# Kernel optimization log

Measured on AMD Instinct MI355X. Metric: run time of the kernel, lower is better.

Reference implementation:

```python
import jax, jax.numpy as jnp
import numpy as np

MERGE_COEFF = 0.5  # fixed beta-merge coefficient (init arg)


def setup_inputs() -> dict:
    key = jax.random.key(0)
    k1, k2, k3, k4 = jax.random.split(key, 4)
    N, M, H = 8192, 8192, 512
    s = 1.0 / np.sqrt(H)
    return {
        "features": jax.random.normal(k1, (N, H), dtype=jnp.float32),
        "memory_features": jax.random.normal(k2, (M, H), dtype=jnp.float32),
        "Wq": jax.random.normal(k3, (H, H), dtype=jnp.float32) * s,
        "bq": jnp.zeros((H,), dtype=jnp.float32),
        "Wk": jax.random.normal(k4, (H, H), dtype=jnp.float32) * s,
        "bk": jnp.zeros((H,), dtype=jnp.float32),
    }


def reference(features, memory_features, Wq, bq, Wk, bk):
    tau = 1.0
    # torch nn.Linear: y = x @ W.T + b
    q = features @ Wq.T + bq                 # [N, H]
    k = memory_features @ Wk.T + bk          # [M, H]
    attn = jax.nn.softmax((q @ k.T) / tau, axis=-1)  # [N, M]
    augment = attn @ memory_features          # [N, H]
    c = MERGE_COEFF
    return c * features + (1.0 - c) * augment
```

## Files before the change

### kernel.cpp

```cpp
#include <hip/hip_runtime.h>


typedef _Float16 half8 __attribute__((ext_vector_type(8)));
typedef _Float16 half4 __attribute__((ext_vector_type(4)));
typedef float floatx4 __attribute__((ext_vector_type(4)));

#define MFMA16(a, b, c) __builtin_amdgcn_mfma_f32_16x16x32_f16((a), (b), (c), 0, 0, 0)

static constexpr int H = 512;
static constexpr int NROWS = 8192;

__device__ __forceinline__ void dma16(half8* lds_dst, const void* g_src) {
    __builtin_amdgcn_global_load_lds(
        (const __attribute__((address_space(1))) unsigned int*)g_src,
        (__attribute__((address_space(3))) unsigned int*)lds_dst,
        16, 0, 0);
}

__global__ void castpack_kernel(const float* __restrict__ F, const float* __restrict__ Mem,
                                const float* __restrict__ wq, const float* __restrict__ wk,
                                _Float16* __restrict__ f16pk, _Float16* __restrict__ m16pk,
                                _Float16* __restrict__ wq16, _Float16* __restrict__ wk16,
                                half8* __restrict__ vp) {
    if (blockIdx.x < 1024) {
        __shared__ _Float16 xl[16 * 520];
        const int t = threadIdx.x;
        const int rowt0 = blockIdx.x * 16;
        const float* src = (rowt0 < 8192) ? (F + (size_t)rowt0 * 512)
                                          : (Mem + (size_t)(rowt0 - 8192) * 512);
        _Float16* dstpk = (rowt0 < 8192) ? f16pk : m16pk;
        const int rowb = blockIdx.x & 511;
#pragma unroll
        for (int i = 0; i < 8; ++i) {
            int li = t + i * 256;
            int r  = li >> 7;
            int c4 = (li & 127) * 4;
            float4 v = *(const float4*)&src[(size_t)r * 512 + c4];
            half4 h;
            h[0] = (_Float16)v.x; h[1] = (_Float16)v.y;
            h[2] = (_Float16)v.z; h[3] = (_Float16)v.w;
            *(half4*)&xl[r * 520 + c4] = h;
        }
        __syncthreads();
        half8* dst = (half8*)dstpk;
#pragma unroll
        for (int i = 0; i < 4; ++i) {
            int u = t + i * 256;
            int j = u >> 4, ri = u & 15;
            half8 v = *(const half8*)&xl[ri * 520 + j * 8];
            dst[(size_t)rowb * 1024 + u] = v;
        }
    } else if (blockIdx.x < 1536) {
        size_t i4 = (size_t)((blockIdx.x - 1024) * 256 + threadIdx.x) * 4;
        const float* src; _Float16* dst; size_t off;
        if (i4 < 262144ull) { src = wq; dst = wq16; off = i4; }
        else                { src = wk; dst = wk16; off = i4 - 262144ull; }
        int col = (int)(off >> 9);
        int in0 = (int)(off & 511);
        float4 v = *(const float4*)&src[off];
        half4 h;
        h[0] = (_Float16)v.x; h[1] = (_Float16)v.y;
        h[2] = (_Float16)v.z; h[3] = (_Float16)v.w;
        _Float16* base = dst + (size_t)((col >> 4) * 8192 + (in0 >> 3) * 128 +
                                        (col & 15) * 8 + ((in0 >> 2) & 1) * 4);
        *(half4*)base = h;
    } else {
        int cid = (blockIdx.x - 1536) * 256 + threadIdx.x;
        int kb  = cid >> 11;
        int rem = cid & 2047;
        int db  = rem >> 6;
        int gc  = rem & 63;
        int g   = gc >> 4, c = gc & 15;
        const float* src = Mem + (size_t)(kb * 32 + g * 8) * H + db * 16 + c;
        half8 v;
#pragma unroll
        for (int j = 0; j < 8; ++j) v[j] = (_Float16)src[(size_t)j * H];
        vp[cid] = v;
    }
}

__global__ __launch_bounds__(256, 4)
void proj_kernel(const _Float16* __restrict__ Xq, const _Float16* __restrict__ Wq16,
                 const float* __restrict__ bq, _Float16* __restrict__ oq,
                 const _Float16* __restrict__ Xk, const _Float16* __restrict__ Wk16,
                 const float* __restrict__ bk, _Float16* __restrict__ ok) {
    const _Float16* X16 = blockIdx.z ? Xk : Xq;
    const _Float16* W16 = blockIdx.z ? Wk16 : Wq16;
    const float*    bias = blockIdx.z ? bk : bq;
    _Float16*       out = blockIdx.z ? ok : oq;

    const int lane = threadIdx.x & 63;
    const int wave = threadIdx.x >> 6;
    const int row0 = blockIdx.x * 128 + wave * 32;
    const int rowb0 = blockIdx.x * 8 + wave * 2;
    const int col0 = blockIdx.y * 64;
    const int colb0 = col0 >> 4;
    const int lr = lane & 15, lq = lane >> 4;

    floatx4 acc[2][4];
#pragma unroll
    for (int rt = 0; rt < 2; ++rt)
#pragma unroll
        for (int nt = 0; nt < 4; ++nt) { acc[rt][nt][0] = 0.f; acc[rt][nt][1] = 0.f; acc[rt][nt][2] = 0.f; acc[rt][nt][3] = 0.f; }

    const half8* xb = (const half8*)X16;
    const half8* wbase = (const half8*)W16;

#pragma unroll
    for (int kk = 0; kk < 16; ++kk) {
        half8 a0 = xb[(size_t)rowb0 * 1024 + kk * 64 + lq * 16 + lr];
        half8 a1 = xb[(size_t)(rowb0 + 1) * 1024 + kk * 64 + lq * 16 + lr];
#pragma unroll
        for (int nt = 0; nt < 4; ++nt) {
            half8 bf = wbase[(size_t)(colb0 + nt) * 1024 + kk * 64 + lq * 16 + lr];
            acc[0][nt] = MFMA16(a0, bf, acc[0][nt]);
            acc[1][nt] = MFMA16(a1, bf, acc[1][nt]);
        }
    }
#pragma unroll
    for (int rt = 0; rt < 2; ++rt)
#pragma unroll
        for (int nt = 0; nt < 4; ++nt) {
            int col = col0 + nt * 16 + lr;
            float b = bias[col];
#pragma unroll
            for (int r = 0; r < 4; ++r) {
                int row = row0 + rt * 16 + lq * 4 + r;
                out[(size_t)row * H + col] = (_Float16)(acc[rt][nt][r] + b);
            }
        }
}

__global__ __launch_bounds__(512, 2)
void flash_kernel(const _Float16* __restrict__ q16, const _Float16* __restrict__ k16,
                  const half8* __restrict__ vp, _Float16* __restrict__ opart,
                  float* __restrict__ mpart, float* __restrict__ lpart) {
    __shared__ half8 klds[2][2048];
    __shared__ half8 vlds[2][2048];
    __shared__ _Float16 plds[2][128 * 36];
    __shared__ float alds[2][128];
    __shared__ float llds[128];
    __shared__ int flagw[2][8];

    const int tid = threadIdx.x;
    const int lane = tid & 63;
    const int wave = tid >> 6;
    const int rbk = blockIdx.x >> 2;
    const int slice = blockIdx.x & 3;
    const int row0 = rbk * 128;
    const int lr = lane & 15, lq = lane >> 4;

    int koff[4];
#pragma unroll
    for (int i = 0; i < 4; ++i) {
        int d = tid + i * 512;
        int c = d >> 10, kk = (d >> 6) & 15, g = (d >> 4) & 3, cc = d & 15;
        koff[i] = c * 8192 + cc * 512 + kk * 32 + g * 8;
    }

    const half8* qrow = (const half8*)(q16 + (size_t)(row0 + wave * 16 + lr) * H);
    half8 qf[16];
#pragma unroll
    for (int kk = 0; kk < 16; ++kk) qf[kk] = qrow[kk * 4 + lq];

    floatx4 o[8][4];
#pragma unroll
    for (int rb = 0; rb < 8; ++rb)
#pragma unroll
        for (int f = 0; f < 4; ++f) { o[rb][f][0] = 0.f; o[rb][f][1] = 0.f; o[rb][f][2] = 0.f; o[rb][f][3] = 0.f; }
    float m[4], l[4];
#pragma unroll
    for (int r = 0; r < 4; ++r) { m[r] = -1e30f; l[r] = 0.f; }

    {
        const int kt0 = slice * 64;
        const _Float16* ksrc0 = k16 + (size_t)kt0 * 16384;
        const half8* vsrc0 = vp + (size_t)kt0 * 2048;
#pragma unroll
        for (int i = 0; i < 4; ++i) dma16(&klds[0][tid + i * 512], ksrc0 + koff[i]);
#pragma unroll
        for (int i = 0; i < 4; ++i) dma16(&vlds[0][tid + i * 512], &vsrc0[tid + i * 512]);
        const _Float16* ksrc1 = k16 + (size_t)(kt0 + 1) * 16384;
#pragma unroll
        for (int i = 0; i < 4; ++i) dma16(&klds[1][tid + i * 512], ksrc1 + koff[i]);
    }

    for (int tt = 0; tt < 64; ++tt) {
        const int b = tt & 1;

        asm volatile("s_waitcnt vmcnt(8) lgkmcnt(0)" ::: "memory");
        __builtin_amdgcn_s_barrier();

        if (tt > 0) {
            const int q1 = b ^ 1;
#pragma unroll
            for (int rb = 0; rb < 8; ++rb) {
                if (flagw[q1][rb]) {
                    float a0 = alds[q1][rb * 16 + lq * 4 + 0];
                    float a1 = alds[q1][rb * 16 + lq * 4 + 1];
                    float a2 = alds[q1][rb * 16 + lq * 4 + 2];
                    float a3 = alds[q1][rb * 16 + lq * 4 + 3];
#pragma unroll
                    for (int f = 0; f < 4; ++f) {
                        o[rb][f][0] *= a0; o[rb][f][1] *= a1;
                        o[rb][f][2] *= a2; o[rb][f][3] *= a3;
                    }
                }
            }
            __builtin_amdgcn_s_setprio(1);
            half8 vf[4];
#pragma unroll
            for (int f = 0; f < 4; ++f) vf[f] = vlds[q1][(wave * 4 + f) * 64 + lane];
#pragma unroll
            for (int rb = 0; rb < 8; ++rb) {
                half8 pfr = *(const half8*)&plds[q1][(rb * 16 + lr) * 36 + lq * 8];
#pragma unroll
                for (int f = 0; f < 4; ++f) o[rb][f] = MFMA16(pfr, vf[f], o[rb][f]);
            }
            __builtin_amdgcn_s_setprio(0);
        }

        __builtin_amdgcn_s_setprio(1);
        floatx4 s0 = {0.f, 0.f, 0.f, 0.f}, s1 = {0.f, 0.f, 0.f, 0.f};
#pragma unroll
        for (int kk = 0; kk < 16; ++kk) {
            s0 = MFMA16(qf[kk], klds[b][kk * 64 + lane], s0);
            s1 = MFMA16(qf[kk], klds[b][1024 + kk * 64 + lane], s1);
        }
        __builtin_amdgcn_s_setprio(0);

        float tm[4]; int trig = 0;
#pragma unroll
        for (int r = 0; r < 4; ++r) {
            tm[r] = fmaxf(s0[r], s1[r]);
            trig |= (tm[r] > m[r] + 10.f) ? 1 : 0;
        }
        const int trigany = __any(trig) ? 1 : 0;
        if (lane == 0) flagw[b][wave] = trigany;
        if (trigany) {
            float al[4];
#pragma unroll
            for (int r = 0; r < 4; ++r) {
                float mx = tm[r];
                mx = fmaxf(mx, __shfl_xor(mx, 1));
                mx = fmaxf(mx, __shfl_xor(mx, 2));
                mx = fmaxf(mx, __shfl_xor(mx, 4));
                mx = fmaxf(mx, __shfl_xor(mx, 8));
                float mn = (mx > m[r] + 10.f) ? mx : m[r];
                al[r] = __expf(m[r] - mn);
                m[r] = mn;
                l[r] *= al[r];
            }
            if (lr == 0) {
#pragma unroll
                for (int r = 0; r < 4; ++r) alds[b][wave * 16 + lq * 4 + r] = al[r];
            }
        }

#pragma unroll
        for (int r = 0; r < 4; ++r) {
            float p0 = __expf(s0[r] - m[r]);
            float p1 = __expf(s1[r] - m[r]);
            l[r] += p0 + p1;
            plds[b][(wave * 16 + lq * 4 + r) * 36 + lr]      = (_Float16)p0;
            plds[b][(wave * 16 + lq * 4 + r) * 36 + 16 + lr] = (_Float16)p1;
        }

        asm volatile("s_waitcnt lgkmcnt(0)" ::: "memory");
        __builtin_amdgcn_s_barrier();

        {
            int vt = tt + 1; if (vt > 63) vt = 63;
            int kt2 = tt + 2; if (kt2 > 63) kt2 = 63;
            const half8* vsrc = vp + (size_t)(slice * 64 + vt) * 2048;
#pragma unroll
            for (int i = 0; i < 4; ++i) dma16(&vlds[(tt + 1) & 1][tid + i * 512], &vsrc[tid + i * 512]);
            const _Float16* ksrc = k16 + (size_t)(slice * 64 + kt2) * 16384;
#pragma unroll
            for (int i = 0; i < 4; ++i) dma16(&klds[b][tid + i * 512], ksrc + koff[i]);
        }
    }

    asm volatile("s_waitcnt lgkmcnt(0)" ::: "memory");
    {
#pragma unroll
        for (int rb = 0; rb < 8; ++rb) {
            if (flagw[1][rb]) {
                float a0 = alds[1][rb * 16 + lq * 4 + 0];
                float a1 = alds[1][rb * 16 + lq * 4 + 1];
                float a2 = alds[1][rb * 16 + lq * 4 + 2];
                float a3 = alds[1][rb * 16 + lq * 4 + 3];
#pragma unroll
                for (int f = 0; f < 4; ++f) {
                    o[rb][f][0] *= a0; o[rb][f][1] *= a1;
                    o[rb][f][2] *= a2; o[rb][f][3] *= a3;
                }
            }
        }
        __builtin_amdgcn_s_setprio(1);
        half8 vf[4];
#pragma unroll
        for (int f = 0; f < 4; ++f) vf[f] = vlds[1][(wave * 4 + f) * 64 + lane];
#pragma unroll
        for (int rb = 0; rb < 8; ++rb) {
            half8 pfr = *(const half8*)&plds[1][(rb * 16 + lr) * 36 + lq * 8];
#pragma unroll
            for (int f = 0; f < 4; ++f) o[rb][f] = MFMA16(pfr, vf[f], o[rb][f]);
        }
        __builtin_amdgcn_s_setprio(0);
    }

#pragma unroll
    for (int r = 0; r < 4; ++r) {
        float lv = l[r];
        lv += __shfl_xor(lv, 1); lv += __shfl_xor(lv, 2);
        lv += __shfl_xor(lv, 4); lv += __shfl_xor(lv, 8);
        l[r] = lv;
    }
    if (lr == 0) {
#pragma unroll
        for (int r = 0; r < 4; ++r) {
            int row = wave * 16 + lq * 4 + r;
            llds[row] = l[r];
            mpart[slice * NROWS + row0 + row] = m[r];
            lpart[slice * NROWS + row0 + row] = l[r];
        }
    }
    __syncthreads();

    _Float16* ob = opart + (size_t)slice * NROWS * H;
#pragma unroll
    for (int rb = 0; rb < 8; ++rb) {
#pragma unroll
        for (int rr = 0; rr < 4; ++rr) {
            float linv = 1.0f / llds[rb * 16 + lq * 4 + rr];
            size_t row = row0 + rb * 16 + lq * 4 + rr;
#pragma unroll
            for (int f = 0; f < 4; ++f)
                ob[row * H + wave * 64 + f * 16 + lr] = (_Float16)(o[rb][f][rr] * linv);
        }
    }
}

__global__ void merge_kernel(const _Float16* __restrict__ opart, const float* __restrict__ mpart,
                             const float* __restrict__ lpart, const float* __restrict__ F,
                             float* __restrict__ out) {
    int gid = blockIdx.x * 256 + threadIdx.x;
    size_t idx4 = (size_t)gid * 4;
    int row = (int)(idx4 >> 9);
    float m0 = mpart[row], m1 = mpart[NROWS + row], m2 = mpart[2 * NROWS + row], m3 = mpart[3 * NROWS + row];
    float ms = fmaxf(fmaxf(m0, m1), fmaxf(m2, m3));
    float w0 = __expf(m0 - ms) * lpart[row];
    float w1 = __expf(m1 - ms) * lpart[NROWS + row];
    float w2 = __expf(m2 - ms) * lpart[2 * NROWS + row];
    float w3 = __expf(m3 - ms) * lpart[3 * NROWS + row];
    float rdenom = 1.0f / (w0 + w1 + w2 + w3);
    size_t stride = (size_t)NROWS * H;
    half4 o0 = *(const half4*)&opart[idx4];
    half4 o1 = *(const half4*)&opart[stride + idx4];
    half4 o2 = *(const half4*)&opart[2 * stride + idx4];
    half4 o3 = *(const half4*)&opart[3 * stride + idx4];
    float4 Fv = *(const float4*)&F[idx4];
    float4 res;
    res.x = 0.5f * Fv.x + 0.5f * ((w0 * (float)o0[0] + w1 * (float)o1[0] + w2 * (float)o2[0] + w3 * (float)o3[0]) * rdenom);
    res.y = 0.5f * Fv.y + 0.5f * ((w0 * (float)o0[1] + w1 * (float)o1[1] + w2 * (float)o2[1] + w3 * (float)o3[1]) * rdenom);
    res.z = 0.5f * Fv.z + 0.5f * ((w0 * (float)o0[2] + w1 * (float)o1[2] + w2 * (float)o2[2] + w3 * (float)o3[2]) * rdenom);
    res.w = 0.5f * Fv.w + 0.5f * ((w0 * (float)o0[3] + w1 * (float)o1[3] + w2 * (float)o2[3] + w3 * (float)o3[3]) * rdenom);
    *(float4*)&out[idx4] = res;
}

extern "C" void kernel_launch(void* const* d_in, const int* in_sizes, int n_in,
                              void* d_out, int out_size, void* d_ws, size_t ws_size,
                              hipStream_t stream) {
    const float* F   = (const float*)d_in[0];
    const float* Mem = (const float*)d_in[1];
    const float* Wq  = (const float*)d_in[2];
    const float* bq  = (const float*)d_in[3];
    const float* Wk  = (const float*)d_in[4];
    const float* bk  = (const float*)d_in[5];
    float* out = (float*)d_out;

    char* ws = (char*)d_ws;
    _Float16* q16   = (_Float16*)(ws);
    _Float16* k16   = (_Float16*)(ws + (8ull << 20));
    half8*    vp    = (half8*)(ws + (16ull << 20));
    _Float16* opart = (_Float16*)(ws + (24ull << 20));
    _Float16* f16pk = (_Float16*)(ws + (24ull << 20));
    _Float16* m16pk = (_Float16*)(ws + (32ull << 20));
    float*    mpart = (float*)(ws + (56ull << 20));
    float*    lpart = (float*)(ws + (56ull << 20) + (128ull << 10));
    _Float16* wq16  = (_Float16*)(ws + (57ull << 20));
    _Float16* wk16  = (_Float16*)(ws + (57ull << 20) + (512ull << 10));

    castpack_kernel<<<3584, 256, 0, stream>>>(F, Mem, Wq, Wk, f16pk, m16pk, wq16, wk16, vp);
    proj_kernel<<<dim3(64, 8, 2), 256, 0, stream>>>(f16pk, wq16, bq, q16, m16pk, wk16, bk, k16);
    flash_kernel<<<256, 512, 0, stream>>>(q16, k16, vp, opart, mpart, lpart);
    merge_kernel<<<4096, 256, 0, stream>>>(opart, mpart, lpart, F, out);
}
```

Baseline: 305.3 us.

## Pre-pack K projection into flash tile layout via LDS-staged epilogue

The projection kernel now stages its output tile in shared memory and writes it with 16-byte vector stores. For Q it writes row-major rows, and for K it writes directly in the packed tile order the flash kernel's LDS DMA expects. The flash kernel then loads K tiles contiguously instead of through a scattered per-thread offset table. This trades a small LDS round trip and barrier in the projection for coalesced stores and contiguous K streaming in the attention loop.

New measurement: 300.3 us, median of 2. No clear change (-1.7%).

```diff
diff --git a/kernel.cpp b/kernel.cpp
--- a/kernel.cpp
+++ b/kernel.cpp
@@ -84,14 +84,16 @@
                  const float* __restrict__ bq, _Float16* __restrict__ oq,
                  const _Float16* __restrict__ Xk, const _Float16* __restrict__ Wk16,
                  const float* __restrict__ bk, _Float16* __restrict__ ok) {
+    __shared__ _Float16 ct[128 * 68];
+
     const _Float16* X16 = blockIdx.z ? Xk : Xq;
     const _Float16* W16 = blockIdx.z ? Wk16 : Wq16;
     const float*    bias = blockIdx.z ? bk : bq;
     _Float16*       out = blockIdx.z ? ok : oq;
 
-    const int lane = threadIdx.x & 63;
-    const int wave = threadIdx.x >> 6;
-    const int row0 = blockIdx.x * 128 + wave * 32;
+    const int t = threadIdx.x;
+    const int lane = t & 63;
+    const int wave = t >> 6;
     const int rowb0 = blockIdx.x * 8 + wave * 2;
     const int col0 = blockIdx.y * 64;
     const int colb0 = col0 >> 4;
@@ -117,22 +119,50 @@
             acc[1][nt] = MFMA16(a1, bf, acc[1][nt]);
         }
     }
-#pragma unroll
-    for (int rt = 0; rt < 2; ++rt)
-#pragma unroll
-        for (int nt = 0; nt < 4; ++nt) {
-            int col = col0 + nt * 16 + lr;
-            float b = bias[col];
+
+#pragma unroll
+    for (int nt = 0; nt < 4; ++nt) {
+        float b = bias[col0 + nt * 16 + lr];
+#pragma unroll
+        for (int rt = 0; rt < 2; ++rt)
 #pragma unroll
             for (int r = 0; r < 4; ++r) {
-                int row = row0 + rt * 16 + lq * 4 + r;
-                out[(size_t)row * H + col] = (_Float16)(acc[rt][nt][r] + b);
-            }
-        }
+                int lrow = wave * 32 + rt * 16 + lq * 4 + r;
+                ct[lrow * 68 + nt * 16 + lr] = (_Float16)(acc[rt][nt][r] + b);
+            }
+    }
+    __syncthreads();
+
+    if (blockIdx.z == 0) {
+        half8* outq = (half8*)out;
+#pragma unroll
+        for (int i = 0; i < 4; ++i) {
+            int u = t + i * 256;
+            int row = u >> 3, c8 = u & 7;
+            half8 v = *(const half8*)&ct[row * 68 + c8 * 8];
+            outq[(size_t)(blockIdx.x * 128 + row) * 64 + (col0 >> 3) + c8] = v;
+        }
+    } else {
+        half8* outk = (half8*)out;
+#pragma unroll
+        for (int i = 0; i < 4; ++i) {
+            int u = t + i * 256;
+            int ktl = u >> 8;
+            int c   = (u >> 7) & 1;
+            int kkl = (u >> 6) & 1;
+            int g   = (u >> 4) & 3;
+            int cc  = u & 15;
+            int lkey = ktl * 32 + c * 16 + cc;
+            int ld   = kkl * 32 + g * 8;
+            half8 v = *(const half8*)&ct[lkey * 68 + ld];
+            outk[(size_t)(blockIdx.x * 4 + ktl) * 2048 + c * 1024 +
+                 ((col0 >> 5) + kkl) * 64 + g * 16 + cc] = v;
+        }
+    }
 }
 
 __global__ __launch_bounds__(512, 2)
-void flash_kernel(const _Float16* __restrict__ q16, const _Float16* __restrict__ k16,
+void flash_kernel(const _Float16* __restrict__ q16, const _Float16* __restrict__ kpk,
                   const half8* __restrict__ vp, _Float16* __restrict__ opart,
                   float* __restrict__ mpart, float* __restrict__ lpart) {
     __shared__ half8 klds[2][2048];
@@ -150,13 +180,7 @@
     const int row0 = rbk * 128;
     const int lr = lane & 15, lq = lane >> 4;
 
-    int koff[4];
-#pragma unroll
-    for (int i = 0; i < 4; ++i) {
-        int d = tid + i * 512;
-        int c = d >> 10, kk = (d >> 6) & 15, g = (d >> 4) & 3, cc = d & 15;
-        koff[i] = c * 8192 + cc * 512 + kk * 32 + g * 8;
-    }
+    const half8* kbase = (const half8*)kpk;
 
     const half8* qrow = (const half8*)(q16 + (size_t)(row0 + wave * 16 + lr) * H);
     half8 qf[16];
@@ -174,15 +198,15 @@
 
     {
         const int kt0 = slice * 64;
-        const _Float16* ksrc0 = k16 + (size_t)kt0 * 16384;
+        const half8* ksrc0 = kbase + (size_t)kt0 * 2048;
         const half8* vsrc0 = vp + (size_t)kt0 * 2048;
 #pragma unroll
-        for (int i = 0; i < 4; ++i) dma16(&klds[0][tid + i * 512], ksrc0 + koff[i]);
+        for (int i = 0; i < 4; ++i) dma16(&klds[0][tid + i * 512], ksrc0 + tid + i * 512);
 #pragma unroll
         for (int i = 0; i < 4; ++i) dma16(&vlds[0][tid + i * 512], &vsrc0[tid + i * 512]);
-        const _Float16* ksrc1 = k16 + (size_t)(kt0 + 1) * 16384;
-#pragma unroll
-        for (int i = 0; i < 4; ++i) dma16(&klds[1][tid + i * 512], ksrc1 + koff[i]);
+        const half8* ksrc1 = kbase + (size_t)(kt0 + 1) * 2048;
+#pragma unroll
+        for (int i = 0; i < 4; ++i) dma16(&klds[1][tid + i * 512], ksrc1 + tid + i * 512);
     }
 
     for (int tt = 0; tt < 64; ++tt) {
@@ -275,9 +299,9 @@
             const half8* vsrc = vp + (size_t)(slice * 64 + vt) * 2048;
 #pragma unroll
             for (int i = 0; i < 4; ++i) dma16(&vlds[(tt + 1) & 1][tid + i * 512], &vsrc[tid + i * 512]);
-            const _Float16* ksrc = k16 + (size_t)(slice * 64 + kt2) * 16384;
-#pragma unroll
-            for (int i = 0; i < 4; ++i) dma16(&klds[b][tid + i * 512], ksrc + koff[i]);
+            const half8* ksrc = kbase + (size_t)(slice * 64 + kt2) * 2048;
+#pragma unroll
+            for (int i = 0; i < 4; ++i) dma16(&klds[b][tid + i * 512], ksrc + tid + i * 512);
         }
     }
 
@@ -382,7 +406,7 @@
 
     char* ws = (char*)d_ws;
     _Float16* q16   = (_Float16*)(ws);
-    _Float16* k16   = (_Float16*)(ws + (8ull << 20));
+    _Float16* kpk   = (_Float16*)(ws + (8ull << 20));
     half8*    vp    = (half8*)(ws + (16ull << 20));
     _Float16* opart = (_Float16*)(ws + (24ull << 20));
     _Float16* f16pk = (_Float16*)(ws + (24ull << 20));
@@ -393,7 +417,7 @@
     _Float16* wk16  = (_Float16*)(ws + (57ull << 20) + (512ull << 10));
 
     castpack_kernel<<<3584, 256, 0, stream>>>(F, Mem, Wq, Wk, f16pk, m16pk, wq16, wk16, vp);
-    proj_kernel<<<dim3(64, 8, 2), 256, 0, stream>>>(f16pk, wq16, bq, q16, m16pk, wk16, bk, k16);
-    flash_kernel<<<256, 512, 0, stream>>>(q16, k16, vp, opart, mpart, lpart);
+    proj_kernel<<<dim3(64, 8, 2), 256, 0, stream>>>(f16pk, wq16, bq, q16, m16pk, wk16, bk, kpk);
+    flash_kernel<<<256, 512, 0, stream>>>(q16, kpk, vp, opart, mpart, lpart);
     merge_kernel<<<4096, 256, 0, stream>>>(opart, mpart, lpart, F, out);
 }
```
